# Kernel optimization log

Hardware: AMD Instinct MI355X
Metric: run time of the kernel (lower is better)

Reference implementation:

```python
import jax, jax.numpy as jnp
from jax import lax
import numpy as np

HID = 1000


def _lstm_cell(x, h, c, W_ih, W_hh, b_ih, b_hh):
    # PyTorch nn.LSTMCell gate order: i, f, g, o
    gates = x @ W_ih.T + b_ih + h @ W_hh.T + b_hh  # [B, 4H]
    i, f, g, o = jnp.split(gates, 4, axis=-1)
    c2 = jax.nn.sigmoid(f) * c + jax.nn.sigmoid(i) * jnp.tanh(g)
    h2 = jax.nn.sigmoid(o) * jnp.tanh(c2)
    return h2, c2


def setup_inputs() -> dict:
    key = jax.random.key(0)
    ks = jax.random.split(key, 8)
    B, T, nbones = 256, 49, 64
    D = nbones * 3
    s = 0.05
    inp = {"enc_in": jax.random.normal(ks[0], (B, T, D), jnp.float32)}
    dims = [D, HID, HID]
    for l in range(3):
        inp[f"W_ih{l}"] = jax.random.normal(ks[1 + 2 * l], (4 * HID, dims[l]), jnp.float32) * s
        inp[f"W_hh{l}"] = jax.random.normal(ks[2 + 2 * l], (4 * HID, HID), jnp.float32) * s
        inp[f"b_ih{l}"] = jnp.zeros((4 * HID,), jnp.float32)
        inp[f"b_hh{l}"] = jnp.zeros((4 * HID,), jnp.float32)
    inp["train"] = 0  # eval mode: dropout is identity
    return inp


def reference(enc_in, W_ih0, W_hh0, b_ih0, b_hh0,
              W_ih1, W_hh1, b_ih1, b_hh1,
              W_ih2, W_hh2, b_ih2, b_hh2, train):
    params = [(W_ih0, W_hh0, b_ih0, b_hh0),
              (W_ih1, W_hh1, b_ih1, b_hh1),
              (W_ih2, W_hh2, b_ih2, b_hh2)]
    B = enc_in.shape[0]
    zeros = jnp.zeros((B, HID), enc_in.dtype)
    init = (tuple(zeros for _ in range(3)), tuple(zeros for _ in range(3)))

    def step(carry, x):
        hs, cs = carry
        new_h, new_c = [], []
        inp = x
        for l in range(3):
            h2, c2 = _lstm_cell(inp, hs[l], cs[l], *params[l])
            new_h.append(h2)
            new_c.append(c2)
            inp = h2  # dropout with train=False is identity
        return (tuple(new_h), tuple(new_c)), jnp.stack(new_h)  # [3, B, H]

    # scan over time: enc_in [B, T, D] -> [T, B, D]
    _, ys = lax.scan(step, init, jnp.transpose(enc_in, (1, 0, 2)))
    # ys: [T, 3, B, H] -> [3, B, T, H]; equals the original per-layer `output`
    out = jnp.transpose(ys, (1, 2, 0, 3))
    return out
```

## Files before the change

kernel.cpp:

```cpp
#include <hip/hip_runtime.h>

#define HID_ 1000
#define NB 256
#define TT 49
#define DIN 192
#define NPAD 1024
#define M_ALL (TT * 256)

typedef _Float16 f16;
typedef _Float16 f16x4 __attribute__((ext_vector_type(4)));
typedef _Float16 f16x8 __attribute__((ext_vector_type(8)));
typedef float f32x4 __attribute__((ext_vector_type(4)));
typedef const __attribute__((address_space(1))) unsigned int* gas_u32;
typedef __attribute__((address_space(3))) unsigned int* las_u32;

__device__ __forceinline__ float sigmf_(float x) {
    return 1.0f / (1.0f + __expf(-x));
}
__device__ __forceinline__ float tanhf_(float x) {
    float ax = fabsf(x);
    float e = __expf(-2.0f * ax);
    float t = (1.0f - e) / (1.0f + e);
    return copysignf(t, x);
}

__global__ __launch_bounds__(256) void conv_weight_v(
    const float* __restrict__ src, f16* __restrict__ dst, int K, int KPADv, int total8) {
    int idx = blockIdx.x * blockDim.x + threadIdx.x;
    if (idx >= total8) return;
    const int kpw = KPADv >> 3;
    const int kp = (idx % kpw) << 3;
    const int rest = idx / kpw;
    const int np = rest & 1023;
    const int g = rest >> 10;
    f16x8 v = {};
    if (np < HID_ && kp < K) {
        const float* sp = src + (size_t)(g * HID_ + np) * K + kp;
        float4 a = *(const float4*)sp;
        float4 b = *(const float4*)(sp + 4);
        v[0] = (f16)a.x; v[1] = (f16)a.y; v[2] = (f16)a.z; v[3] = (f16)a.w;
        v[4] = (f16)b.x; v[5] = (f16)b.y; v[6] = (f16)b.z; v[7] = (f16)b.w;
    }
    *(f16x8*)(dst + (size_t)rest * KPADv + kp) = v;
}

__global__ __launch_bounds__(256) void conv_x_v(
    const float* __restrict__ src, f16* __restrict__ dst, int total8) {
    int idx = blockIdx.x * blockDim.x + threadIdx.x;
    if (idx >= total8) return;
    const int kp = (idx % (DIN / 8)) << 3;
    const int rest = idx / (DIN / 8);
    const int b = rest & 255;
    const int t = rest >> 8;
    const float* sp = src + ((size_t)b * TT + t) * DIN + kp;
    float4 a = *(const float4*)sp;
    float4 c = *(const float4*)(sp + 4);
    f16x8 v;
    v[0] = (f16)a.x; v[1] = (f16)a.y; v[2] = (f16)a.z; v[3] = (f16)a.w;
    v[4] = (f16)c.x; v[5] = (f16)c.y; v[6] = (f16)c.z; v[7] = (f16)c.w;
    *(f16x8*)(dst + (size_t)rest * DIN + kp) = v;
}

__global__ void conv_bias(const float* __restrict__ bih, const float* __restrict__ bhh,
                          float* __restrict__ dst) {
    int idx = blockIdx.x * blockDim.x + threadIdx.x;
    if (idx < 4 * NPAD) {
        int np = idx & (NPAD - 1);
        int g = idx >> 10;
        float v = 0.0f;
        if (np < HID_) v = bih[g * HID_ + np] + bhh[g * HID_ + np];
        dst[idx] = v;
    }
}

__global__ __launch_bounds__(256) void input_gemm(
    const f16* __restrict__ A, int lda, int kiters,
    const f16* __restrict__ W, int ldw,
    const float* __restrict__ bias,
    f16* __restrict__ pre2) {
    __shared__ f16 As[128 * 64];
    __shared__ f16 Bs[128 * 64];
    const int id = blockIdx.x;
    const int sw = (id & 7) * (gridDim.x >> 3) + (id >> 3);
    const int m0 = (sw >> 5) << 7;
    const int n0 = (sw & 31) << 7;
    const int w = threadIdx.x >> 6;
    const int lane = threadIdx.x & 63;
    const int r = lane & 15;
    const int u = lane >> 4;
    const int kb8 = u << 3;
    const int wm = (w >> 1) << 6, wn = (w & 1) << 6;
    const int strow = (w << 5) + (lane >> 3);
    const int stcol = (lane & 7) << 3;

    f32x4 acc[4][4];
#pragma unroll
    for (int i = 0; i < 4; i++)
#pragma unroll
        for (int j = 0; j < 4; j++) acc[i][j] = (f32x4){0.f, 0.f, 0.f, 0.f};

    for (int kt = 0; kt < kiters; kt++) {
        const int k0 = kt << 6;
#pragma unroll
        for (int q = 0; q < 4; q++) {
            const int row = strow + (q << 3);
            const int cbase = ((w << 5) + (q << 3)) << 6;
            const f16* ga = A + (size_t)(m0 + row) * lda + k0 + stcol;
            const f16* gb = W + (size_t)(n0 + row) * ldw + k0 + stcol;
            __builtin_amdgcn_global_load_lds((gas_u32)ga, (las_u32)(As + cbase), 16, 0, 0);
            __builtin_amdgcn_global_load_lds((gas_u32)gb, (las_u32)(Bs + cbase), 16, 0, 0);
        }
        __syncthreads();
#pragma unroll
        for (int ks = 0; ks < 2; ks++) {
            f16x8 av[4], bv[4];
#pragma unroll
            for (int i = 0; i < 4; i++)
                av[i] = *(const f16x8*)(As + ((wm + i * 16 + r) << 6) + (ks << 5) + kb8);
#pragma unroll
            for (int j = 0; j < 4; j++)
                bv[j] = *(const f16x8*)(Bs + ((wn + j * 16 + r) << 6) + (ks << 5) + kb8);
#pragma unroll
            for (int i = 0; i < 4; i++)
#pragma unroll
                for (int j = 0; j < 4; j++)
                    acc[i][j] = __builtin_amdgcn_mfma_f32_16x16x32_f16(av[i], bv[j], acc[i][j], 0, 0, 0);
        }
        __syncthreads();
    }

#pragma unroll
    for (int j = 0; j < 4; j++) {
        const int gcol = n0 + wn + j * 16 + r;
        const float bj = bias[gcol];
        const int g = gcol >> 10, cl = gcol & 1023;
        const int jt2 = cl >> 5, c = cl & 31;
        const int n2 = c >> 4, r2 = c & 15;
        const int l2 = u * 16 + r2;
#pragma unroll
        for (int i = 0; i < 4; i++) {
            const int grow = m0 + wm + i * 16 + (u << 2);
            const int t_ = grow >> 8;
            const int bt2 = (grow >> 5) & 7;
            const int mi = i & 1;
            f16x4 hv;
#pragma unroll
            for (int q = 0; q < 4; q++) hv[q] = (f16)(acc[i][j][q] + bj);
            *(f16x4*)(pre2 + ((((size_t)t_ * 8 + bt2) * 32 + jt2) * 4 + g) * 1024 +
                      l2 * 16 + mi * 8 + n2 * 4) = hv;
        }
    }
}

__global__ __launch_bounds__(512, 2) void rec_persist(
    const f16* __restrict__ Whh, const f16* __restrict__ pre2,
    f16* __restrict__ hall, float* __restrict__ outl,
    unsigned int* __restrict__ flags) {
    __shared__ __align__(16) char smem[64 * 1024];
    __shared__ float pl[2 * 4 * 32 * 34];
    const int bid = blockIdx.x;
    const int bt = bid & 7;
    const int jt = bid >> 3;
    const int b0 = bt << 5;
    const int jc0 = jt << 5;
    const int tid = threadIdx.x;
    const int w = tid >> 6;
    const int g = w >> 1;
    const int kh = w & 1;
    const int lane = tid & 63;
    const int r = lane & 15;
    const int u = lane >> 4;
    const int kbb = u << 4;
    const int rbase = u << 2;
    const int swz = (r & 7) << 4;

    f16x8 wreg[2][16];
#pragma unroll
    for (int n = 0; n < 2; n++) {
        const f16* wp = Whh + ((size_t)(g * NPAD + jc0 + n * 16 + r)) * NPAD + (kh << 9) + (u << 3);
#pragma unroll
        for (int ks = 0; ks < 16; ks++) wreg[n][ks] = *(const f16x8*)(wp + ks * 32);
    }

    const int eb = tid >> 4;
    const int ej = (tid & 15) << 1;
    float cv[2] = {0.f, 0.f};
    unsigned int* myflags = flags + bt * TT;
    const size_t preblk = ((((size_t)bt) * 32 + jt) * 4 + g) * 1024 + lane * 16;

    auto LOADP = [&](int tindex, f16x8& pa, f16x8& pb) {
        if (kh == 0) {
            const f16* pp = pre2 + (size_t)tindex * 8 * 32 * 4 * 1024 + preblk;
            pa = *(const f16x8*)pp;
            pb = *(const f16x8*)(pp + 8);
        }
    };

    auto STEP = [&](int t, f16x8& pc0, f16x8& pc1, f16x8& pn0, f16x8& pn1) {
        LOADP(t + 1 < TT ? t + 1 : t, pn0, pn1);

        if (t > 0) {
            while (__hip_atomic_load(myflags + (t - 1), __ATOMIC_RELAXED,
                                     __HIP_MEMORY_SCOPE_AGENT) < 32u) {}
            asm volatile("" ::: "memory");
            const f16* hread = hall + (size_t)(t - 1) * NB * NPAD;
#pragma unroll
            for (int i = 0; i < 8; i++) {
                int c = tid + (i << 9);
                int row = c >> 7;
                int cb = (c & 127) << 4;
                f16x8 v = *(const f16x8*)(hread + (size_t)(b0 + row) * NPAD + (cb >> 1));
                *(f16x8*)(smem + row * 2048 + (cb ^ ((row & 7) << 4))) = v;
            }
        }
        __syncthreads();

        f32x4 acc[2][2];
#pragma unroll
        for (int mi = 0; mi < 2; mi++)
#pragma unroll
            for (int n = 0; n < 2; n++)
#pragma unroll
                for (int q = 0; q < 4; q++) {
                    if (kh == 0)
                        acc[mi][n][q] = (float)(mi == 0 ? pc0[n * 4 + q] : pc1[n * 4 + q]);
                    else
                        acc[mi][n][q] = 0.f;
                }

        if (t > 0) {
#pragma unroll
            for (int ks = 0; ks < 16; ks++) {
                const int ksg = (kh << 4) + ks;
                f16x8 a0 = *(const f16x8*)(smem + r * 2048 + ((ksg * 64 + kbb) ^ swz));
                f16x8 a1 = *(const f16x8*)(smem + (16 + r) * 2048 + ((ksg * 64 + kbb) ^ swz));
                acc[0][0] = __builtin_amdgcn_mfma_f32_16x16x32_f16(a0, wreg[0][ks], acc[0][0], 0, 0, 0);
                acc[0][1] = __builtin_amdgcn_mfma_f32_16x16x32_f16(a0, wreg[1][ks], acc[0][1], 0, 0, 0);
                acc[1][0] = __builtin_amdgcn_mfma_f32_16x16x32_f16(a1, wreg[0][ks], acc[1][0], 0, 0, 0);
                acc[1][1] = __builtin_amdgcn_mfma_f32_16x16x32_f16(a1, wreg[1][ks], acc[1][1], 0, 0, 0);
            }
        }

#pragma unroll
        for (int mi = 0; mi < 2; mi++)
#pragma unroll
            for (int n = 0; n < 2; n++)
#pragma unroll
                for (int q = 0; q < 4; q++)
                    pl[((kh * 4 + g) * 32 + mi * 16 + rbase + q) * 34 + n * 16 + r] =
                        acc[mi][n][q];
        __syncthreads();

        float hvv[2];
        {
            float gv[4][2];
#pragma unroll
            for (int gate = 0; gate < 4; gate++) {
                float2 p0 = *(const float2*)&pl[((0 * 4 + gate) * 32 + eb) * 34 + ej];
                float2 p1 = *(const float2*)&pl[((1 * 4 + gate) * 32 + eb) * 34 + ej];
                gv[gate][0] = p0.x + p1.x;
                gv[gate][1] = p0.y + p1.y;
            }
#pragma unroll
            for (int q = 0; q < 2; q++) {
                float cn = sigmf_(gv[1][q]) * cv[q] + sigmf_(gv[0][q]) * tanhf_(gv[2][q]);
                hvv[q] = sigmf_(gv[3][q]) * tanhf_(cn);
                cv[q] = cn;
            }
        }
        {
            union { f16 h2[2]; unsigned uu; } cvt;
            cvt.h2[0] = (f16)hvv[0];
            cvt.h2[1] = (f16)hvv[1];
            __hip_atomic_store(
                (unsigned*)(hall + ((size_t)t * NB + b0 + eb) * NPAD + jc0 + ej), cvt.uu,
                __ATOMIC_RELAXED, __HIP_MEMORY_SCOPE_AGENT);
        }
        __syncthreads();
        if (tid == 0)
            __hip_atomic_fetch_add(myflags + t, 1u, __ATOMIC_RELAXED, __HIP_MEMORY_SCOPE_AGENT);
        const int col = jc0 + ej;
        if (col < HID_) {
            *(float2*)(outl + ((size_t)(b0 + eb) * TT + t) * HID_ + col) =
                make_float2(hvv[0], hvv[1]);
        }
    };

    f16x8 pA0 = {}, pA1 = {}, pB0 = {}, pB1 = {};
    LOADP(0, pA0, pA1);
    for (int t = 0; t < TT; t += 2) {
        STEP(t, pA0, pA1, pB0, pB1);
        if (t + 1 < TT) STEP(t + 1, pB0, pB1, pA0, pA1);
    }
}

extern "C" void kernel_launch(void* const* d_in, const int* in_sizes, int n_in,
                              void* d_out, int out_size, void* d_ws, size_t ws_size,
                              hipStream_t stream) {
    const float* enc_in = (const float*)d_in[0];
    const float* W_ih[3] = {(const float*)d_in[1], (const float*)d_in[5], (const float*)d_in[9]};
    const float* W_hh[3] = {(const float*)d_in[2], (const float*)d_in[6], (const float*)d_in[10]};
    const float* b_ih[3] = {(const float*)d_in[3], (const float*)d_in[7], (const float*)d_in[11]};
    const float* b_hh[3] = {(const float*)d_in[4], (const float*)d_in[8], (const float*)d_in[12]};
    float* out = (float*)d_out;

    char* ws = (char*)d_ws;
    size_t off = 0;
    auto alloc = [&](size_t bytes) {
        char* p = ws + off;
        off += (bytes + 255) & ~(size_t)255;
        return p;
    };
    f16* Wih_c[3];
    f16* Whh_c[3];
    Wih_c[0] = (f16*)alloc(4ull * NPAD * DIN * sizeof(f16));
    Whh_c[0] = (f16*)alloc(4ull * NPAD * NPAD * sizeof(f16));
    Wih_c[1] = (f16*)alloc(4ull * NPAD * NPAD * sizeof(f16));
    Whh_c[1] = (f16*)alloc(4ull * NPAD * NPAD * sizeof(f16));
    Wih_c[2] = (f16*)alloc(4ull * NPAD * NPAD * sizeof(f16));
    Whh_c[2] = (f16*)alloc(4ull * NPAD * NPAD * sizeof(f16));
    float* bias_c[3];
    for (int l = 0; l < 3; l++) bias_c[l] = (float*)alloc(4ull * NPAD * sizeof(float));
    f16* xbf = (f16*)alloc((size_t)TT * NB * DIN * sizeof(f16));
    f16* hall[3];
    for (int l = 0; l < 3; l++) hall[l] = (f16*)alloc((size_t)TT * NB * NPAD * sizeof(f16));
    f16* pre2 = (f16*)alloc((size_t)M_ALL * 4096 * sizeof(f16));
    unsigned int* flags = (unsigned int*)alloc(3ull * 8 * TT * sizeof(unsigned int));

    hipMemsetAsync(flags, 0, 3ull * 8 * TT * sizeof(unsigned int), stream);

    {
        int t8_l0 = 4 * NPAD * DIN / 8;
        conv_weight_v<<<(t8_l0 + 255) / 256, 256, 0, stream>>>(W_ih[0], Wih_c[0], DIN, DIN, t8_l0);
        int t8 = 4 * NPAD * NPAD / 8;
        conv_weight_v<<<(t8 + 255) / 256, 256, 0, stream>>>(W_hh[0], Whh_c[0], HID_, NPAD, t8);
        conv_weight_v<<<(t8 + 255) / 256, 256, 0, stream>>>(W_ih[1], Wih_c[1], HID_, NPAD, t8);
        conv_weight_v<<<(t8 + 255) / 256, 256, 0, stream>>>(W_hh[1], Whh_c[1], HID_, NPAD, t8);
        conv_weight_v<<<(t8 + 255) / 256, 256, 0, stream>>>(W_ih[2], Wih_c[2], HID_, NPAD, t8);
        conv_weight_v<<<(t8 + 255) / 256, 256, 0, stream>>>(W_hh[2], Whh_c[2], HID_, NPAD, t8);
    }
    {
        int t8x = TT * NB * (DIN / 8);
        conv_x_v<<<(t8x + 255) / 256, 256, 0, stream>>>(enc_in, xbf, t8x);
    }
    for (int l = 0; l < 3; l++)
        conv_bias<<<(4 * NPAD + 255) / 256, 256, 0, stream>>>(b_ih[l], b_hh[l], bias_c[l]);

    for (int l = 0; l < 3; l++) {
        if (l == 0)
            input_gemm<<<3136, 256, 0, stream>>>(xbf, DIN, DIN / 64, Wih_c[0], DIN,
                                                 bias_c[0], pre2);
        else
            input_gemm<<<3136, 256, 0, stream>>>(hall[l - 1], NPAD, NPAD / 64, Wih_c[l], NPAD,
                                                 bias_c[l], pre2);
        rec_persist<<<256, 512, 0, stream>>>(
            Whh_c[l], pre2, hall[l], out + (size_t)l * NB * TT * HID_,
            flags + (size_t)l * 8 * TT);
    }
}
```

Before: 1.097 ms.

## Split each block's batch tile into two independent 16-row chains and interleave them

Each persistent recurrent block now processes two independent 16-row batch chunks with separate flags, shared-memory buffers and cell states, alternating phases between them. The aim is to let one chunk's wait on other blocks' h from the previous step overlap with compute on the other chunk, shortening the dependency stall per step. The input GEMM's pre-activation layout and the flag layout are changed to match 16-row chunks. The cost is twice as many barriers and flag spins per timestep, half the MFMA work per phase, and narrower 16-bit atomic stores.

```diff
diff --git a/kernel.cpp b/kernel.cpp
--- a/kernel.cpp
+++ b/kernel.cpp
@@ -136,18 +136,16 @@
         const int g = gcol >> 10, cl = gcol & 1023;
         const int jt2 = cl >> 5, c = cl & 31;
         const int n2 = c >> 4, r2 = c & 15;
-        const int l2 = u * 16 + r2;
 #pragma unroll
         for (int i = 0; i < 4; i++) {
             const int grow = m0 + wm + i * 16 + (u << 2);
             const int t_ = grow >> 8;
-            const int bt2 = (grow >> 5) & 7;
-            const int mi = i & 1;
+            const int ch = (grow >> 4) & 15;
             f16x4 hv;
 #pragma unroll
             for (int q = 0; q < 4; q++) hv[q] = (f16)(acc[i][j][q] + bj);
-            *(f16x4*)(pre2 + ((((size_t)t_ * 8 + bt2) * 32 + jt2) * 4 + g) * 1024 +
-                      l2 * 16 + mi * 8 + n2 * 4) = hv;
+            *(f16x4*)(pre2 + ((((size_t)t_ * 16 + ch) * 32 + jt2) * 4 + g) * 512 +
+                      (u * 16 + r2) * 8 + n2 * 4) = hv;
         }
     }
 }
@@ -156,12 +154,13 @@
     const f16* __restrict__ Whh, const f16* __restrict__ pre2,
     f16* __restrict__ hall, float* __restrict__ outl,
     unsigned int* __restrict__ flags) {
-    __shared__ __align__(16) char smem[64 * 1024];
-    __shared__ float pl[2 * 4 * 32 * 34];
+    __shared__ __align__(16) char hA[16 * 2048];
+    __shared__ __align__(16) char hB[16 * 2048];
+    __shared__ float pl[2 * 4 * 16 * 34];
     const int bid = blockIdx.x;
-    const int bt = bid & 7;
+    const int c = bid & 7;
     const int jt = bid >> 3;
-    const int b0 = bt << 5;
+    const int chA = 2 * c, chB = 2 * c + 1;
     const int jc0 = jt << 5;
     const int tid = threadIdx.x;
     const int w = tid >> 6;
@@ -171,7 +170,6 @@
     const int r = lane & 15;
     const int u = lane >> 4;
     const int kbb = u << 4;
-    const int rbase = u << 2;
     const int swz = (r & 7) << 4;
 
     f16x8 wreg[2][16];
@@ -182,115 +180,99 @@
         for (int ks = 0; ks < 16; ks++) wreg[n][ks] = *(const f16x8*)(wp + ks * 32);
     }
 
-    const int eb = tid >> 4;
-    const int ej = (tid & 15) << 1;
-    float cv[2] = {0.f, 0.f};
-    unsigned int* myflags = flags + bt * TT;
-    const size_t preblk = ((((size_t)bt) * 32 + jt) * 4 + g) * 1024 + lane * 16;
-
-    auto LOADP = [&](int tindex, f16x8& pa, f16x8& pb) {
-        if (kh == 0) {
-            const f16* pp = pre2 + (size_t)tindex * 8 * 32 * 4 * 1024 + preblk;
-            pa = *(const f16x8*)pp;
-            pb = *(const f16x8*)(pp + 8);
-        }
+    const int eb = tid >> 5;
+    const int ej = tid & 31;
+    float cvA = 0.f, cvB = 0.f;
+    unsigned int* flA = flags + chA * 64;
+    unsigned int* flB = flags + chB * 64;
+    const size_t preblkA = (((size_t)chA * 32 + jt) * 4 + g) * 512 + lane * 8;
+    const size_t preblkB = (((size_t)chB * 32 + jt) * 4 + g) * 512 + lane * 8;
+
+    auto LOADP = [&](int tindex, size_t preblk, f16x8& pc) {
+        if (kh == 0) pc = *(const f16x8*)(pre2 + (size_t)tindex * 1048576 + preblk);
     };
 
-    auto STEP = [&](int t, f16x8& pc0, f16x8& pc1, f16x8& pn0, f16x8& pn1) {
-        LOADP(t + 1 < TT ? t + 1 : t, pn0, pn1);
-
+    auto PHASE = [&](int t, int ch, char* hX, unsigned int* fl, f16x8& pc, float& cv) {
         if (t > 0) {
-            while (__hip_atomic_load(myflags + (t - 1), __ATOMIC_RELAXED,
+            while (__hip_atomic_load(fl + (t - 1), __ATOMIC_RELAXED,
                                      __HIP_MEMORY_SCOPE_AGENT) < 32u) {}
             asm volatile("" ::: "memory");
-            const f16* hread = hall + (size_t)(t - 1) * NB * NPAD;
-#pragma unroll
-            for (int i = 0; i < 8; i++) {
-                int c = tid + (i << 9);
-                int row = c >> 7;
-                int cb = (c & 127) << 4;
-                f16x8 v = *(const f16x8*)(hread + (size_t)(b0 + row) * NPAD + (cb >> 1));
-                *(f16x8*)(smem + row * 2048 + (cb ^ ((row & 7) << 4))) = v;
+            const char* hread = (const char*)(hall + (size_t)(t - 1) * NB * NPAD +
+                                              (size_t)ch * 16 * NPAD);
+#pragma unroll
+            for (int i = 0; i < 4; i++) {
+                int c2 = tid + (i << 9);
+                int row = c2 >> 7;
+                int cb = (c2 & 127) << 4;
+                f16x8 v = *(const f16x8*)(hread + (size_t)row * 2048 + cb);
+                *(f16x8*)(hX + row * 2048 + (cb ^ ((row & 7) << 4))) = v;
             }
         }
         __syncthreads();
 
-        f32x4 acc[2][2];
-#pragma unroll
-        for (int mi = 0; mi < 2; mi++)
-#pragma unroll
-            for (int n = 0; n < 2; n++)
-#pragma unroll
-                for (int q = 0; q < 4; q++) {
-                    if (kh == 0)
-                        acc[mi][n][q] = (float)(mi == 0 ? pc0[n * 4 + q] : pc1[n * 4 + q]);
-                    else
-                        acc[mi][n][q] = 0.f;
-                }
+        f32x4 acc[2];
+#pragma unroll
+        for (int n = 0; n < 2; n++)
+#pragma unroll
+            for (int q = 0; q < 4; q++)
+                acc[n][q] = (kh == 0) ? (float)pc[n * 4 + q] : 0.f;
 
         if (t > 0) {
 #pragma unroll
             for (int ks = 0; ks < 16; ks++) {
                 const int ksg = (kh << 4) + ks;
-                f16x8 a0 = *(const f16x8*)(smem + r * 2048 + ((ksg * 64 + kbb) ^ swz));
-                f16x8 a1 = *(const f16x8*)(smem + (16 + r) * 2048 + ((ksg * 64 + kbb) ^ swz));
-                acc[0][0] = __builtin_amdgcn_mfma_f32_16x16x32_f16(a0, wreg[0][ks], acc[0][0], 0, 0, 0);
-                acc[0][1] = __builtin_amdgcn_mfma_f32_16x16x32_f16(a0, wreg[1][ks], acc[0][1], 0, 0, 0);
-                acc[1][0] = __builtin_amdgcn_mfma_f32_16x16x32_f16(a1, wreg[0][ks], acc[1][0], 0, 0, 0);
-                acc[1][1] = __builtin_amdgcn_mfma_f32_16x16x32_f16(a1, wreg[1][ks], acc[1][1], 0, 0, 0);
+                f16x8 a0 = *(const f16x8*)(hX + r * 2048 + ((ksg * 64 + kbb) ^ swz));
+                acc[0] = __builtin_amdgcn_mfma_f32_16x16x32_f16(a0, wreg[0][ks], acc[0], 0, 0, 0);
+                acc[1] = __builtin_amdgcn_mfma_f32_16x16x32_f16(a0, wreg[1][ks], acc[1], 0, 0, 0);
             }
         }
-
-#pragma unroll
-        for (int mi = 0; mi < 2; mi++)
-#pragma unroll
-            for (int n = 0; n < 2; n++)
-#pragma unroll
-                for (int q = 0; q < 4; q++)
-                    pl[((kh * 4 + g) * 32 + mi * 16 + rbase + q) * 34 + n * 16 + r] =
-                        acc[mi][n][q];
-        __syncthreads();
-
-        float hvv[2];
+#pragma unroll
+        for (int n = 0; n < 2; n++)
+#pragma unroll
+            for (int q = 0; q < 4; q++)
+                pl[((kh * 4 + g) * 16 + u * 4 + q) * 34 + n * 16 + r] = acc[n][q];
+        __syncthreads();
+
+        float gv[4];
+#pragma unroll
+        for (int gate = 0; gate < 4; gate++)
+            gv[gate] = pl[((0 * 4 + gate) * 16 + eb) * 34 + ej] +
+                       pl[((1 * 4 + gate) * 16 + eb) * 34 + ej];
+        float cn = sigmf_(gv[1]) * cv + sigmf_(gv[0]) * tanhf_(gv[2]);
+        float hv = sigmf_(gv[3]) * tanhf_(cn);
+        cv = cn;
         {
-            float gv[4][2];
-#pragma unroll
-            for (int gate = 0; gate < 4; gate++) {
-                float2 p0 = *(const float2*)&pl[((0 * 4 + gate) * 32 + eb) * 34 + ej];
-                float2 p1 = *(const float2*)&pl[((1 * 4 + gate) * 32 + eb) * 34 + ej];
-                gv[gate][0] = p0.x + p1.x;
-                gv[gate][1] = p0.y + p1.y;
-            }
-#pragma unroll
-            for (int q = 0; q < 2; q++) {
-                float cn = sigmf_(gv[1][q]) * cv[q] + sigmf_(gv[0][q]) * tanhf_(gv[2][q]);
-                hvv[q] = sigmf_(gv[3][q]) * tanhf_(cn);
-                cv[q] = cn;
-            }
-        }
-        {
-            union { f16 h2[2]; unsigned uu; } cvt;
-            cvt.h2[0] = (f16)hvv[0];
-            cvt.h2[1] = (f16)hvv[1];
+            union { f16 h; unsigned short s; } cvt;
+            cvt.h = (f16)hv;
             __hip_atomic_store(
-                (unsigned*)(hall + ((size_t)t * NB + b0 + eb) * NPAD + jc0 + ej), cvt.uu,
-                __ATOMIC_RELAXED, __HIP_MEMORY_SCOPE_AGENT);
+                (unsigned short*)(hall + (size_t)t * NB * NPAD +
+                                  (size_t)(ch * 16 + eb) * NPAD + jc0 + ej),
+                cvt.s, __ATOMIC_RELAXED, __HIP_MEMORY_SCOPE_AGENT);
         }
         __syncthreads();
         if (tid == 0)
-            __hip_atomic_fetch_add(myflags + t, 1u, __ATOMIC_RELAXED, __HIP_MEMORY_SCOPE_AGENT);
+            __hip_atomic_fetch_add(fl + t, 1u, __ATOMIC_RELAXED, __HIP_MEMORY_SCOPE_AGENT);
         const int col = jc0 + ej;
-        if (col < HID_) {
-            *(float2*)(outl + ((size_t)(b0 + eb) * TT + t) * HID_ + col) =
-                make_float2(hvv[0], hvv[1]);
-        }
+        if (col < HID_)
+            outl[((size_t)(ch * 16 + eb) * TT + t) * HID_ + col] = hv;
     };
 
-    f16x8 pA0 = {}, pA1 = {}, pB0 = {}, pB1 = {};
-    LOADP(0, pA0, pA1);
+    f16x8 pcA = {}, pnA = {}, pcB = {}, pnB = {};
+    LOADP(0, preblkA, pcA);
+    LOADP(0, preblkB, pcB);
     for (int t = 0; t < TT; t += 2) {
-        STEP(t, pA0, pA1, pB0, pB1);
-        if (t + 1 < TT) STEP(t + 1, pB0, pB1, pA0, pA1);
+        const int t1 = (t + 1 < TT) ? t + 1 : t;
+        const int t2 = (t + 2 < TT) ? t + 2 : t;
+        LOADP(t1, preblkA, pnA);
+        LOADP(t1, preblkB, pnB);
+        PHASE(t, chA, hA, flA, pcA, cvA);
+        PHASE(t, chB, hB, flB, pcB, cvB);
+        if (t + 1 < TT) {
+            LOADP(t2, preblkA, pcA);
+            LOADP(t2, preblkB, pcB);
+            PHASE(t + 1, chA, hA, flA, pnA, cvA);
+            PHASE(t + 1, chB, hB, flB, pnB, cvB);
+        }
     }
 }
 
@@ -325,9 +307,10 @@
     f16* hall[3];
     for (int l = 0; l < 3; l++) hall[l] = (f16*)alloc((size_t)TT * NB * NPAD * sizeof(f16));
     f16* pre2 = (f16*)alloc((size_t)M_ALL * 4096 * sizeof(f16));
-    unsigned int* flags = (unsigned int*)alloc(3ull * 8 * TT * sizeof(unsigned int));
-
-    hipMemsetAsync(flags, 0, 3ull * 8 * TT * sizeof(unsigned int), stream);
+    const size_t fl_layer = 16 * 64;
+    unsigned int* flags = (unsigned int*)alloc(3 * fl_layer * sizeof(unsigned int));
+
+    hipMemsetAsync(flags, 0, 3 * fl_layer * sizeof(unsigned int), stream);
 
     {
         int t8_l0 = 4 * NPAD * DIN / 8;
@@ -355,6 +338,6 @@
                                                  bias_c[l], pre2);
         rec_persist<<<256, 512, 0, stream>>>(
             Whh_c[l], pre2, hall[l], out + (size_t)l * NB * TT * HID_,
-            flags + (size_t)l * 8 * TT);
-    }
-}
+            flags + (size_t)l * fl_layer);
+    }
+}
```

Result: slower. 1.126 ms (+2.7%).
